# Kernel tuning notes

Hardware: AMD Instinct MI355X
Metric: run time of the kernel (lower is better)

Reference implementation:

```python
import jax, jax.numpy as jnp
import numpy as np

NUM_HEADS = 16

def setup_inputs() -> dict:
    key = jax.random.key(0)
    k1, k2, k3 = jax.random.split(key, 3)
    B, S, H = 2, 2048, 1024
    x = jax.random.normal(k1, (B, S, H), dtype=jnp.float32)
    w_qkv = jax.random.normal(k2, (H, 3 * H), dtype=jnp.float32) * (1.0 / np.sqrt(H))
    w_out = jax.random.normal(k3, (H, H), dtype=jnp.float32) * (1.0 / np.sqrt(H))
    return {"x": x, "w_qkv": w_qkv, "w_out": w_out}

def reference(x, w_qkv, w_out):
    B, S, H = x.shape
    nh = NUM_HEADS
    dh = H // nh
    qkv = x @ w_qkv  # (B, S, 3H)
    q, k, v = jnp.split(qkv, 3, axis=-1)
    # (B, nh, S, dh)
    q = q.reshape(B, S, nh, dh).transpose(0, 2, 1, 3)
    k = k.reshape(B, S, nh, dh).transpose(0, 2, 1, 3)
    v = v.reshape(B, S, nh, dh).transpose(0, 2, 1, 3)
    att = jnp.einsum('bhsd,bhSd->bhsS', q, k) / np.sqrt(dh).astype(np.float32)
    causal = jnp.tril(jnp.ones((S, S), dtype=bool))
    att = jnp.where(causal[None, None], att, -jnp.inf)
    att = jax.nn.softmax(att, axis=-1)
    out = jnp.einsum('bhsS,bhSd->bhsd', att, v)
    out = out.transpose(0, 2, 1, 3).reshape(B, S, H)
    return out @ w_out
```

## Files before the change

kernel.cpp:

```cpp
#include <hip/hip_runtime.h>

#define DEVINL __device__ __forceinline__

typedef __attribute__((ext_vector_type(8)))  __bf16         bf16x8;
typedef __attribute__((ext_vector_type(4)))  float          f32x4;
typedef __attribute__((ext_vector_type(16))) float          f32x16;
typedef __attribute__((ext_vector_type(8)))  unsigned short ushort8;
typedef __attribute__((ext_vector_type(4)))  unsigned short ushort4v;
typedef __attribute__((ext_vector_type(4)))  unsigned int   uint4v;
typedef __attribute__((ext_vector_type(4)))  float          float4v;

DEVINL unsigned short f2bf(float f) {
  unsigned int u = __float_as_uint(f);
  u += 0x7fffu + ((u >> 16) & 1u);
  return (unsigned short)(u >> 16);
}

DEVINL bf16x8 ldbf8(const unsigned short* p) {
  return __builtin_bit_cast(bf16x8, *(const ushort8*)p);
}

DEVINL unsigned cvtpk_bf16(float lo, float hi) {
  unsigned r;
  asm("v_cvt_pk_bf16_f32 %0, %1, %2" : "=v"(r) : "v"(lo), "v"(hi));
  return r;
}

DEVINL void gload_lds16(const unsigned short* g, unsigned short* l) {
  __builtin_amdgcn_global_load_lds((const __attribute__((address_space(1))) void*)g,
                                   (__attribute__((address_space(3))) void*)l, 16, 0, 0);
}

__global__ __launch_bounds__(256) void cvt_f32_bf16_kernel(
    const float* __restrict__ in, unsigned short* __restrict__ out, int n4) {
  int i = blockIdx.x * 256 + threadIdx.x;
  const int stride = gridDim.x * 256;
  for (; i < n4; i += stride) {
    float4v v = *(const float4v*)(in + (size_t)4 * i);
    ushort4v o;
    o[0] = f2bf(v[0]); o[1] = f2bf(v[1]); o[2] = f2bf(v[2]); o[3] = f2bf(v[3]);
    *(ushort4v*)(out + (size_t)4 * i) = o;
  }
}

__global__ __launch_bounds__(256) void transpose_cvt_kernel(
    const float* __restrict__ in, unsigned short* __restrict__ out, int R, int C) {
  __shared__ float tile[32][33];
  const int tx = threadIdx.x & 31, ty = threadIdx.x >> 5;
  const int r0 = blockIdx.y << 5, c0 = blockIdx.x << 5;
#pragma unroll
  for (int i = 0; i < 32; i += 8)
    tile[ty + i][tx] = in[(size_t)(r0 + ty + i) * C + (c0 + tx)];
  __syncthreads();
#pragma unroll
  for (int i = 0; i < 32; i += 8)
    out[(size_t)(c0 + ty + i) * R + (r0 + tx)] = f2bf(tile[tx][ty + i]);
}

__global__ __launch_bounds__(256) void v_transpose_kernel(
    const unsigned short* __restrict__ qkv, unsigned short* __restrict__ VtG) {
  const int S = 2048, LD = 3072;
  const int s0 = blockIdx.x << 5;
  const int bh = blockIdx.y;
  const int b = bh >> 4, h = bh & 15;
  __shared__ __align__(16) unsigned short T[32][72];
  const int t = threadIdx.x;
  {
    const int s = t >> 3, d0 = (t & 7) << 3;
    *(ushort8*)&T[s][d0] =
        *(const ushort8*)(qkv + ((size_t)(b * S) + s0 + s) * LD + 2048 + h * 64 + d0);
  }
  __syncthreads();
  {
    const int d = t >> 2, sc = (t & 3) << 3;
    ushort8 o;
#pragma unroll
    for (int e = 0; e < 8; ++e) o[e] = T[sc + e][d];
    *(ushort8*)(VtG + ((size_t)bh * 64 + d) * S + s0 + sc) = o;
  }
}

template <bool OUT_BF16>
__global__ __launch_bounds__(256) void gemm_bt_kernel(
    const unsigned short* __restrict__ A,
    const unsigned short* __restrict__ Bt,
    void* __restrict__ Cout,
    int M, int N, int K, int lda, int ldb, int ldc) {
  __shared__ __align__(16) unsigned short As[128 * 32];
  __shared__ __align__(16) unsigned short Bs[128 * 32];
  const int tid = threadIdx.x;
  const int lane = tid & 63, wave = tid >> 6;
  const int wr = wave >> 1, wc = wave & 1;
  const int g = lane >> 4, q = lane & 15;
  const int row0 = blockIdx.x << 7, col0 = blockIdx.y << 7;

  const int srow = tid >> 2, skcol = (tid & 3) << 3;
  const unsigned short* Ap0 = A + (size_t)(row0 + srow) * lda + skcol;
  const unsigned short* Ap1 = Ap0 + (size_t)64 * lda;
  const unsigned short* Bp0 = Bt + (size_t)(col0 + srow) * ldb + skcol;
  const unsigned short* Bp1 = Bp0 + (size_t)64 * ldb;
  unsigned short* Asw = As + wave * 512;
  unsigned short* Bsw = Bs + wave * 512;

  f32x4 acc[4][4] = {};

  for (int k0 = 0; k0 < K; k0 += 32) {
    __syncthreads();
    gload_lds16(Ap0, Asw);
    gload_lds16(Ap1, Asw + 2048);
    gload_lds16(Bp0, Bsw);
    gload_lds16(Bp1, Bsw + 2048);
    Ap0 += 32; Ap1 += 32; Bp0 += 32; Bp1 += 32;
    __syncthreads();

    bf16x8 af[4], bfr[4];
#pragma unroll
    for (int mb = 0; mb < 4; ++mb)
      af[mb] = ldbf8(As + (wr * 64 + mb * 16 + q) * 32 + g * 8);
#pragma unroll
    for (int nb = 0; nb < 4; ++nb)
      bfr[nb] = ldbf8(Bs + (wc * 64 + nb * 16 + q) * 32 + g * 8);
#pragma unroll
    for (int mb = 0; mb < 4; ++mb)
#pragma unroll
      for (int nb = 0; nb < 4; ++nb)
        acc[mb][nb] = __builtin_amdgcn_mfma_f32_16x16x32_bf16(af[mb], bfr[nb], acc[mb][nb], 0, 0, 0);
  }

#pragma unroll
  for (int mb = 0; mb < 4; ++mb)
#pragma unroll
    for (int nb = 0; nb < 4; ++nb)
#pragma unroll
      for (int r = 0; r < 4; ++r) {
        const int row = row0 + wr * 64 + mb * 16 + g * 4 + r;
        const int col = col0 + wc * 64 + nb * 16 + q;
        const float v = acc[mb][nb][r];
        if (OUT_BF16) ((unsigned short*)Cout)[(size_t)row * ldc + col] = f2bf(v);
        else          ((float*)Cout)[(size_t)row * ldc + col] = v;
      }
}

__global__ __launch_bounds__(256, 2) void attn_kernel(
    const unsigned short* __restrict__ qkv,
    const unsigned short* __restrict__ VtG,
    unsigned short* __restrict__ O) {
  const int S = 2048, H = 1024, LD = 3072;
  const int wave = threadIdx.x >> 6, lane = threadIdx.x & 63;
  const int c = lane & 31, hh = lane >> 5;

  const int L = blockIdx.x;
  const int member = L >> 8, r0_ = L & 255;
  const int pairid = r0_ & 7, bh = r0_ >> 3;
  const int qc = member ? (15 - pairid) : pairid;
  const int b = bh >> 4, h = bh & 15;
  const int q0w = qc * 128 + wave * 32;

  const unsigned short* Qb = qkv + (size_t)b * S * LD + h * 64;
  const unsigned short* Kb = Qb + H;
  const unsigned short* Vt = VtG + (size_t)(b * 16 + h) * 64 * S;

  __shared__ __align__(16) unsigned short Ks[2][64 * 64];
  __shared__ __align__(16) unsigned short Vs[2][64 * 64];

  const int srow = lane >> 3;
  const int srcg = ((lane & 7) ^ srow) << 3;
  const int wrow = wave * 8 + srow;

  gload_lds16(Kb + (size_t)wrow * LD + srcg,        Ks[0] + wave * 512);
  gload_lds16(Kb + (size_t)(32 + wrow) * LD + srcg, Ks[0] + 2048 + wave * 512);
  gload_lds16(Vt + (size_t)wrow * S + srcg,         Vs[0] + wave * 512);
  gload_lds16(Vt + (size_t)(32 + wrow) * S + srcg,  Vs[0] + 2048 + wave * 512);

  bf16x8 qf[4];
#pragma unroll
  for (int kc = 0; kc < 4; ++kc)
    qf[kc] = ldbf8(Qb + (size_t)(q0w + c) * LD + kc * 16 + hh * 8);

  f32x16 acc[2] = {};
  float m_r = -1e30f, l_r = 0.f;
  const float CE = 0.125f * 1.44269504f;

  const int ntb = qc * 2 + 2;
  int cur = 0;
  const int swz = (c & 7) << 3;

  for (int t = 0; t < ntb; ++t) {
    if (t + 1 < ntb) {
      const int c1 = (t + 1) << 6;
      unsigned short* KsN = Ks[cur ^ 1];
      unsigned short* VsN = Vs[cur ^ 1];
      gload_lds16(Kb + (size_t)(c1 + wrow) * LD + srcg,      KsN + wave * 512);
      gload_lds16(Kb + (size_t)(c1 + 32 + wrow) * LD + srcg, KsN + 2048 + wave * 512);
      gload_lds16(Vt + (size_t)wrow * S + c1 + srcg,         VsN + wave * 512);
      gload_lds16(Vt + (size_t)(32 + wrow) * S + c1 + srcg,  VsN + 2048 + wave * 512);
      asm volatile("s_waitcnt vmcnt(4)" ::: "memory");
    } else {
      asm volatile("s_waitcnt vmcnt(0)" ::: "memory");
    }
    __builtin_amdgcn_s_barrier();

    const int c0 = t << 6;
    const unsigned short* KsC = Ks[cur];
    const unsigned short* VsC = Vs[cur];

    if (c0 <= q0w + 31) {
      int nv = ((q0w + 31 - c0) >> 5) + 1; if (nv > 2) nv = 2;

      bf16x8 kf[2][4];
#pragma unroll
      for (int n = 0; n < 2; ++n) if (n < nv)
#pragma unroll
        for (int kc = 0; kc < 4; ++kc)
          kf[n][kc] = ldbf8(KsC + (n * 32 + c) * 64 + ((kc * 16 + hh * 8) ^ swz));

      f32x16 st[2] = {};
#pragma unroll
      for (int n = 0; n < 2; ++n) if (n < nv)
#pragma unroll
        for (int kc = 0; kc < 4; ++kc)
          st[n] = __builtin_amdgcn_mfma_f32_32x32x16_bf16(kf[n][kc], qf[kc], st[n], 0, 0, 0);

      bf16x8 vf[2][4];
#pragma unroll
      for (int db = 0; db < 2; ++db)
#pragma unroll
        for (int kk = 0; kk < 4; ++kk) if (kk < 2 * nv)
          vf[db][kk] = ldbf8(VsC + (db * 32 + c) * 64 + ((kk * 16 + hh * 8) ^ swz));

      if (c0 + 63 > q0w) {
#pragma unroll
        for (int n = 0; n < 2; ++n) if (n < nv)
#pragma unroll
          for (int r = 0; r < 16; ++r) {
            const int kv = c0 + n * 32 + (r & 3) + 8 * (r >> 2) + 4 * hh;
            if (kv > q0w + c) st[n][r] = -1e30f;
          }
      }

      float pmax = -1e30f;
#pragma unroll
      for (int n = 0; n < 2; ++n) if (n < nv)
#pragma unroll
        for (int r = 0; r < 16; ++r) pmax = fmaxf(pmax, st[n][r]);
      if (!__all(pmax <= m_r + 64.f)) {
        pmax = fmaxf(pmax, __shfl_xor(pmax, 32));
        const float mn = fmaxf(m_r, pmax);
        const float sf = __builtin_amdgcn_exp2f((m_r - mn) * CE);
        m_r = mn; l_r *= sf;
#pragma unroll
        for (int db = 0; db < 2; ++db) acc[db] *= sf;
      }
      const float mC = m_r * CE;
#pragma unroll
      for (int n = 0; n < 2; ++n) if (n < nv)
#pragma unroll
        for (int r = 0; r < 16; ++r) {
          const float p = __builtin_amdgcn_exp2f(fmaf(st[n][r], CE, -mC));
          st[n][r] = p;
          l_r += p;
        }

      bf16x8 pa[4];
#pragma unroll
      for (int n = 0; n < 2; ++n) if (n < nv) {
        unsigned T0 = cvtpk_bf16(st[n][0],  st[n][1]);
        unsigned T1 = cvtpk_bf16(st[n][2],  st[n][3]);
        unsigned T2 = cvtpk_bf16(st[n][4],  st[n][5]);
        unsigned T3 = cvtpk_bf16(st[n][6],  st[n][7]);
        unsigned T4 = cvtpk_bf16(st[n][8],  st[n][9]);
        unsigned T5 = cvtpk_bf16(st[n][10], st[n][11]);
        unsigned T6 = cvtpk_bf16(st[n][12], st[n][13]);
        unsigned T7 = cvtpk_bf16(st[n][14], st[n][15]);
        asm("v_permlane32_swap_b32 %0, %1" : "+v"(T0), "+v"(T2));
        asm("v_permlane32_swap_b32 %0, %1" : "+v"(T1), "+v"(T3));
        asm("v_permlane32_swap_b32 %0, %1" : "+v"(T4), "+v"(T6));
        asm("v_permlane32_swap_b32 %0, %1" : "+v"(T5), "+v"(T7));
        uint4v w0; w0[0] = T0; w0[1] = T1; w0[2] = T2; w0[3] = T3;
        uint4v w1; w1[0] = T4; w1[1] = T5; w1[2] = T6; w1[3] = T7;
        pa[2 * n]     = __builtin_bit_cast(bf16x8, w0);
        pa[2 * n + 1] = __builtin_bit_cast(bf16x8, w1);
      }

#pragma unroll
      for (int kk = 0; kk < 4; ++kk) if (kk < 2 * nv)
#pragma unroll
        for (int db = 0; db < 2; ++db)
          acc[db] = __builtin_amdgcn_mfma_f32_32x32x16_bf16(vf[db][kk], pa[kk], acc[db], 0, 0, 0);
    }

    __builtin_amdgcn_s_barrier();
    cur ^= 1;
  }

  const float lt = l_r + __shfl_xor(l_r, 32);
  const float inv = 1.f / lt;
  const size_t rowbase = (size_t)(b * S + q0w + c) * H + h * 64;
#pragma unroll
  for (int db = 0; db < 2; ++db)
#pragma unroll
    for (int blk = 0; blk < 4; ++blk) {
      ushort4v o;
#pragma unroll
      for (int j = 0; j < 4; ++j) o[j] = f2bf(acc[db][blk * 4 + j] * inv);
      *(ushort4v*)(O + rowbase + db * 32 + blk * 8 + hh * 4) = o;
    }
}

extern "C" void kernel_launch(void* const* d_in, const int* in_sizes, int n_in,
                              void* d_out, int out_size, void* d_ws, size_t ws_size,
                              hipStream_t stream) {
  const float* x     = (const float*)d_in[0];
  const float* w_qkv = (const float*)d_in[1];
  const float* w_out = (const float*)d_in[2];
  const int B = 2, S = 2048, H = 1024;
  const int M = B * S;

  unsigned short* xb    = (unsigned short*)d_ws;
  unsigned short* wqkvT = xb + (size_t)M * H;
  unsigned short* woutT = wqkvT + (size_t)3 * H * H;
  unsigned short* qkvb  = woutT + (size_t)H * H;
  unsigned short* Ob    = qkvb + (size_t)M * 3 * H;
  unsigned short* VtG   = xb;

  cvt_f32_bf16_kernel<<<1024, 256, 0, stream>>>(x, xb, (M * H) / 4);
  transpose_cvt_kernel<<<dim3((3 * H) / 32, H / 32), 256, 0, stream>>>(w_qkv, wqkvT, H, 3 * H);
  transpose_cvt_kernel<<<dim3(H / 32, H / 32), 256, 0, stream>>>(w_out, woutT, H, H);

  gemm_bt_kernel<true><<<dim3(M / 128, (3 * H) / 128), 256, 0, stream>>>(
      xb, wqkvT, qkvb, M, 3 * H, H, H, H, 3 * H);

  v_transpose_kernel<<<dim3(S / 32, 32), 256, 0, stream>>>(qkvb, VtG);

  attn_kernel<<<512, 256, 0, stream>>>(qkvb, VtG, Ob);

  gemm_bt_kernel<false><<<dim3(M / 128, H / 128), 256, 0, stream>>>(
      Ob, woutT, d_out, M, H, H, H, H, H);
}
```

Baseline: 138.6 us.

## Software-pipeline attention loop: overlap QK^T of next tile with softmax/PV of previous

Restructures the flash-attention KV loop so each iteration issues the QK^T MFMAs and V fragment loads for the current tile, then runs the softmax, bf16 packing and PV MFMAs for the previous tile held in registers. This lets the MFMA unit work on the next score tile while the VALU does exp and reduction work, hiding the dependency between matmul and softmax. It also splits the max and sum reductions into four partial accumulators to shorten the dependency chains. The cost is much higher register pressure from carrying the previous scores and V fragments, which may reduce occupancy or cause spills.

```diff
diff --git a/kernel.cpp b/kernel.cpp
--- a/kernel.cpp
+++ b/kernel.cpp
@@ -181,6 +181,66 @@
   float m_r = -1e30f, l_r = 0.f;
   const float CE = 0.125f * 1.44269504f;
 
+  f32x16 stp[2];
+  bf16x8 vfp[2][4];
+  int nvp = 0;
+  bool havePrev = false;
+
+  auto do_prev = [&]() {
+    f32x4 pm = {-1e30f, -1e30f, -1e30f, -1e30f};
+#pragma unroll
+    for (int n = 0; n < 2; ++n) if (n < nvp)
+#pragma unroll
+      for (int r = 0; r < 16; ++r) pm[r & 3] = fmaxf(pm[r & 3], stp[n][r]);
+    const float pmax = fmaxf(fmaxf(pm[0], pm[1]), fmaxf(pm[2], pm[3]));
+    if (!__all(pmax <= m_r + 64.f)) {
+      float px = fmaxf(pmax, __shfl_xor(pmax, 32));
+      const float mn = fmaxf(m_r, px);
+      const float sf = __builtin_amdgcn_exp2f((m_r - mn) * CE);
+      m_r = mn; l_r *= sf;
+#pragma unroll
+      for (int db = 0; db < 2; ++db) acc[db] *= sf;
+    }
+    const float mC = m_r * CE;
+    f32x4 la = {0.f, 0.f, 0.f, 0.f};
+#pragma unroll
+    for (int n = 0; n < 2; ++n) if (n < nvp)
+#pragma unroll
+      for (int r = 0; r < 16; ++r) {
+        const float p = __builtin_amdgcn_exp2f(fmaf(stp[n][r], CE, -mC));
+        stp[n][r] = p;
+        la[r & 3] += p;
+      }
+    l_r += (la[0] + la[1]) + (la[2] + la[3]);
+
+    bf16x8 pa[4];
+#pragma unroll
+    for (int n = 0; n < 2; ++n) if (n < nvp) {
+      unsigned T0 = cvtpk_bf16(stp[n][0],  stp[n][1]);
+      unsigned T1 = cvtpk_bf16(stp[n][2],  stp[n][3]);
+      unsigned T2 = cvtpk_bf16(stp[n][4],  stp[n][5]);
+      unsigned T3 = cvtpk_bf16(stp[n][6],  stp[n][7]);
+      unsigned T4 = cvtpk_bf16(stp[n][8],  stp[n][9]);
+      unsigned T5 = cvtpk_bf16(stp[n][10], stp[n][11]);
+      unsigned T6 = cvtpk_bf16(stp[n][12], stp[n][13]);
+      unsigned T7 = cvtpk_bf16(stp[n][14], stp[n][15]);
+      asm("v_permlane32_swap_b32 %0, %1" : "+v"(T0), "+v"(T2));
+      asm("v_permlane32_swap_b32 %0, %1" : "+v"(T1), "+v"(T3));
+      asm("v_permlane32_swap_b32 %0, %1" : "+v"(T4), "+v"(T6));
+      asm("v_permlane32_swap_b32 %0, %1" : "+v"(T5), "+v"(T7));
+      uint4v w0; w0[0] = T0; w0[1] = T1; w0[2] = T2; w0[3] = T3;
+      uint4v w1; w1[0] = T4; w1[1] = T5; w1[2] = T6; w1[3] = T7;
+      pa[2 * n]     = __builtin_bit_cast(bf16x8, w0);
+      pa[2 * n + 1] = __builtin_bit_cast(bf16x8, w1);
+    }
+
+#pragma unroll
+    for (int kk = 0; kk < 4; ++kk) if (kk < 2 * nvp)
+#pragma unroll
+      for (int db = 0; db < 2; ++db)
+        acc[db] = __builtin_amdgcn_mfma_f32_32x32x16_bf16(vfp[db][kk], pa[kk], acc[db], 0, 0, 0);
+  };
+
   const int ntb = qc * 2 + 2;
   int cur = 0;
   const int swz = (c & 7) << 3;
@@ -203,9 +263,14 @@
     const int c0 = t << 6;
     const unsigned short* KsC = Ks[cur];
     const unsigned short* VsC = Vs[cur];
-
-    if (c0 <= q0w + 31) {
-      int nv = ((q0w + 31 - c0) >> 5) + 1; if (nv > 2) nv = 2;
+    const bool act = (c0 <= q0w + 31);
+
+    f32x16 stc[2] = {};
+    bf16x8 vfc[2][4];
+    int nv = 0;
+
+    if (act) {
+      nv = ((q0w + 31 - c0) >> 5) + 1; if (nv > 2) nv = 2;
 
       bf16x8 kf[2][4];
 #pragma unroll
@@ -214,84 +279,45 @@
         for (int kc = 0; kc < 4; ++kc)
           kf[n][kc] = ldbf8(KsC + (n * 32 + c) * 64 + ((kc * 16 + hh * 8) ^ swz));
 
-      f32x16 st[2] = {};
 #pragma unroll
       for (int n = 0; n < 2; ++n) if (n < nv)
 #pragma unroll
         for (int kc = 0; kc < 4; ++kc)
-          st[n] = __builtin_amdgcn_mfma_f32_32x32x16_bf16(kf[n][kc], qf[kc], st[n], 0, 0, 0);
-
-      bf16x8 vf[2][4];
+          stc[n] = __builtin_amdgcn_mfma_f32_32x32x16_bf16(kf[n][kc], qf[kc], stc[n], 0, 0, 0);
+
 #pragma unroll
       for (int db = 0; db < 2; ++db)
 #pragma unroll
         for (int kk = 0; kk < 4; ++kk) if (kk < 2 * nv)
-          vf[db][kk] = ldbf8(VsC + (db * 32 + c) * 64 + ((kk * 16 + hh * 8) ^ swz));
-
+          vfc[db][kk] = ldbf8(VsC + (db * 32 + c) * 64 + ((kk * 16 + hh * 8) ^ swz));
+    }
+
+    if (havePrev) { do_prev(); havePrev = false; }
+
+    if (act) {
       if (c0 + 63 > q0w) {
 #pragma unroll
         for (int n = 0; n < 2; ++n) if (n < nv)
 #pragma unroll
           for (int r = 0; r < 16; ++r) {
             const int kv = c0 + n * 32 + (r & 3) + 8 * (r >> 2) + 4 * hh;
-            if (kv > q0w + c) st[n][r] = -1e30f;
+            if (kv > q0w + c) stc[n][r] = -1e30f;
           }
       }
-
-      float pmax = -1e30f;
-#pragma unroll
-      for (int n = 0; n < 2; ++n) if (n < nv)
-#pragma unroll
-        for (int r = 0; r < 16; ++r) pmax = fmaxf(pmax, st[n][r]);
-      if (!__all(pmax <= m_r + 64.f)) {
-        pmax = fmaxf(pmax, __shfl_xor(pmax, 32));
-        const float mn = fmaxf(m_r, pmax);
-        const float sf = __builtin_amdgcn_exp2f((m_r - mn) * CE);
-        m_r = mn; l_r *= sf;
-#pragma unroll
-        for (int db = 0; db < 2; ++db) acc[db] *= sf;
-      }
-      const float mC = m_r * CE;
-#pragma unroll
-      for (int n = 0; n < 2; ++n) if (n < nv)
-#pragma unroll
-        for (int r = 0; r < 16; ++r) {
-          const float p = __builtin_amdgcn_exp2f(fmaf(st[n][r], CE, -mC));
-          st[n][r] = p;
-          l_r += p;
-        }
-
-      bf16x8 pa[4];
-#pragma unroll
-      for (int n = 0; n < 2; ++n) if (n < nv) {
-        unsigned T0 = cvtpk_bf16(st[n][0],  st[n][1]);
-        unsigned T1 = cvtpk_bf16(st[n][2],  st[n][3]);
-        unsigned T2 = cvtpk_bf16(st[n][4],  st[n][5]);
-        unsigned T3 = cvtpk_bf16(st[n][6],  st[n][7]);
-        unsigned T4 = cvtpk_bf16(st[n][8],  st[n][9]);
-        unsigned T5 = cvtpk_bf16(st[n][10], st[n][11]);
-        unsigned T6 = cvtpk_bf16(st[n][12], st[n][13]);
-        unsigned T7 = cvtpk_bf16(st[n][14], st[n][15]);
-        asm("v_permlane32_swap_b32 %0, %1" : "+v"(T0), "+v"(T2));
-        asm("v_permlane32_swap_b32 %0, %1" : "+v"(T1), "+v"(T3));
-        asm("v_permlane32_swap_b32 %0, %1" : "+v"(T4), "+v"(T6));
-        asm("v_permlane32_swap_b32 %0, %1" : "+v"(T5), "+v"(T7));
-        uint4v w0; w0[0] = T0; w0[1] = T1; w0[2] = T2; w0[3] = T3;
-        uint4v w1; w1[0] = T4; w1[1] = T5; w1[2] = T6; w1[3] = T7;
-        pa[2 * n]     = __builtin_bit_cast(bf16x8, w0);
-        pa[2 * n + 1] = __builtin_bit_cast(bf16x8, w1);
-      }
-
-#pragma unroll
-      for (int kk = 0; kk < 4; ++kk) if (kk < 2 * nv)
-#pragma unroll
-        for (int db = 0; db < 2; ++db)
-          acc[db] = __builtin_amdgcn_mfma_f32_32x32x16_bf16(vf[db][kk], pa[kk], acc[db], 0, 0, 0);
+      stp[0] = stc[0]; stp[1] = stc[1];
+#pragma unroll
+      for (int db = 0; db < 2; ++db)
+#pragma unroll
+        for (int kk = 0; kk < 4; ++kk) vfp[db][kk] = vfc[db][kk];
+      nvp = nv;
+      havePrev = true;
     }
 
     __builtin_amdgcn_s_barrier();
     cur ^= 1;
   }
+
+  if (havePrev) do_prev();
 
   const float lt = l_r + __shfl_xor(l_r, 32);
   const float inv = 1.f / lt;
```

New measurement: 144.8 us. 4.5% more time.

## Double-buffer GEMM LDS tiles with async prefetch and XOR swizzle

Applied to the files above, without the earlier changes.

Converts the bf16 GEMM main loop to a double-buffered pipeline: the next K-slice is fetched with global-to-LDS loads while MFMAs run on the current buffer, with vmcnt waits replacing the two full syncthreads. LDS columns are XOR-swizzled by row to cut bank conflicts on fragment reads, and launch bounds request three blocks per CU. This doubles shared memory per block and relies on hand-placed waitcnt and barrier ordering being correct.

```diff
diff --git a/kernel.cpp b/kernel.cpp
--- a/kernel.cpp
+++ b/kernel.cpp
@@ -81,50 +81,65 @@
 }
 
 template <bool OUT_BF16>
-__global__ __launch_bounds__(256) void gemm_bt_kernel(
+__global__ __launch_bounds__(256, 3) void gemm_bt_kernel(
     const unsigned short* __restrict__ A,
     const unsigned short* __restrict__ Bt,
     void* __restrict__ Cout,
     int M, int N, int K, int lda, int ldb, int ldc) {
-  __shared__ __align__(16) unsigned short As[128 * 32];
-  __shared__ __align__(16) unsigned short Bs[128 * 32];
+  __shared__ __align__(16) unsigned short As[2][128 * 32];
+  __shared__ __align__(16) unsigned short Bs[2][128 * 32];
   const int tid = threadIdx.x;
   const int lane = tid & 63, wave = tid >> 6;
   const int wr = wave >> 1, wc = wave & 1;
   const int g = lane >> 4, q = lane & 15;
   const int row0 = blockIdx.x << 7, col0 = blockIdx.y << 7;
 
-  const int srow = tid >> 2, skcol = (tid & 3) << 3;
-  const unsigned short* Ap0 = A + (size_t)(row0 + srow) * lda + skcol;
+  const int srow = tid >> 2;
+  const int sg = ((tid & 3) ^ (srow & 3)) << 3;
+  const unsigned short* Ap0 = A + (size_t)(row0 + srow) * lda + sg;
   const unsigned short* Ap1 = Ap0 + (size_t)64 * lda;
-  const unsigned short* Bp0 = Bt + (size_t)(col0 + srow) * ldb + skcol;
+  const unsigned short* Bp0 = Bt + (size_t)(col0 + srow) * ldb + sg;
   const unsigned short* Bp1 = Bp0 + (size_t)64 * ldb;
-  unsigned short* Asw = As + wave * 512;
-  unsigned short* Bsw = Bs + wave * 512;
 
   f32x4 acc[4][4] = {};
 
-  for (int k0 = 0; k0 < K; k0 += 32) {
-    __syncthreads();
-    gload_lds16(Ap0, Asw);
-    gload_lds16(Ap1, Asw + 2048);
-    gload_lds16(Bp0, Bsw);
-    gload_lds16(Bp1, Bsw + 2048);
-    Ap0 += 32; Ap1 += 32; Bp0 += 32; Bp1 += 32;
-    __syncthreads();
+  gload_lds16(Ap0, &As[0][wave * 512]);
+  gload_lds16(Ap1, &As[0][2048 + wave * 512]);
+  gload_lds16(Bp0, &Bs[0][wave * 512]);
+  gload_lds16(Bp1, &Bs[0][2048 + wave * 512]);
+
+  const int gx = (g ^ (q & 3)) << 3;
+  const int nk = K >> 5;
+  int cur = 0;
+
+  for (int t = 0; t < nk; ++t) {
+    if (t + 1 < nk) {
+      Ap0 += 32; Ap1 += 32; Bp0 += 32; Bp1 += 32;
+      gload_lds16(Ap0, &As[cur ^ 1][wave * 512]);
+      gload_lds16(Ap1, &As[cur ^ 1][2048 + wave * 512]);
+      gload_lds16(Bp0, &Bs[cur ^ 1][wave * 512]);
+      gload_lds16(Bp1, &Bs[cur ^ 1][2048 + wave * 512]);
+      asm volatile("s_waitcnt vmcnt(4)" ::: "memory");
+    } else {
+      asm volatile("s_waitcnt vmcnt(0)" ::: "memory");
+    }
+    __builtin_amdgcn_s_barrier();
 
     bf16x8 af[4], bfr[4];
 #pragma unroll
     for (int mb = 0; mb < 4; ++mb)
-      af[mb] = ldbf8(As + (wr * 64 + mb * 16 + q) * 32 + g * 8);
+      af[mb] = ldbf8(&As[cur][(wr * 64 + mb * 16 + q) * 32] + gx);
 #pragma unroll
     for (int nb = 0; nb < 4; ++nb)
-      bfr[nb] = ldbf8(Bs + (wc * 64 + nb * 16 + q) * 32 + g * 8);
+      bfr[nb] = ldbf8(&Bs[cur][(wc * 64 + nb * 16 + q) * 32] + gx);
 #pragma unroll
     for (int mb = 0; mb < 4; ++mb)
 #pragma unroll
       for (int nb = 0; nb < 4; ++nb)
         acc[mb][nb] = __builtin_amdgcn_mfma_f32_16x16x32_bf16(af[mb], bfr[nb], acc[mb][nb], 0, 0, 0);
+
+    __builtin_amdgcn_s_barrier();
+    cur ^= 1;
   }
 
 #pragma unroll
```

After: 131.2 us. 1.06x faster.
